# Kernel tuning notes

Hardware: AMD Instinct MI355X
Metric: run time of the kernel (lower is better)

## Reference

```python
import jax, jax.numpy as jnp
import numpy as np

B, N, E, DIN = 2048, 38, 4, 9
H0, H1, L0 = 256, 256, 512
EPS = 1e-5
_mask_np = np.ones((N, DIN), np.float32)
_mask_np[np.arange(0, N, 2), :] = 0.0
MASK = jnp.asarray(_mask_np)  # (N, DIN); masked rows zeroed


def _bn_relu(h, g, b):
    # h: (B, N, 1, D); BatchNorm2d(N) normalizes over (batch, H=1, W=D) per node channel
    mu = jnp.mean(h, axis=(0, 2, 3), keepdims=True)
    var = jnp.var(h, axis=(0, 2, 3), keepdims=True)  # biased var, as torch BN
    h = (h - mu) * jax.lax.rsqrt(var + EPS) * g[None, :, None, None] + b[None, :, None, None]
    return jax.nn.relu(h)


def _gconv(adj, nodes, Ws, bs, We, be):
    # adj: (B, E, N, N); nodes: (B, N, 1, Din)
    out = Ws.shape[0]
    hs = nodes @ Ws.T + bs  # self term: (B, N, 1, out)
    m = (nodes @ We.T + be).reshape(nodes.shape[0], N, out, E)
    hr = jnp.einsum('bemn,bnce->bmc', adj, m)  # relational aggregation
    return hs + hr[:, :, None, :]


def _forward(adj, x, cWs0, cbs0, cWe0, cbe0, cg0, cb0, cWs1, cbs1, cWe1, cbe1, cg1, cb1, lW0, lb0, lg0, lbb0, fW, fb):
    masked_x = MASK * x
    h = masked_x[:, :, None, :]
    h = _bn_relu(_gconv(adj, h, cWs0, cbs0, cWe0, cbe0), cg0, cb0)
    h = _bn_relu(_gconv(adj, h, cWs1, cbs1, cWe1, cbe1), cg1, cb1)
    h = _bn_relu(h @ lW0.T + lb0, lg0, lbb0)
    h = (h @ fW.T + fb)[:, :, 0, :]  # (B, N, 2*DIN)
    s_logits, t = h[..., :DIN], h[..., DIN:]
    s = jax.nn.sigmoid(s_logits)
    out = masked_x + (1.0 - MASK) * (x + t) * s
    logdet = jnp.sum(jax.nn.log_sigmoid(s_logits).reshape(x.shape[0], -1), axis=1)
    return out, logdet


def setup_inputs() -> dict:
    key = jax.random.key(0)
    ks = jax.random.split(key, 8)
    rn = lambda k, shape: jax.random.normal(ks[k], shape, jnp.float32) * 0.1
    return {
        'adj': jax.random.uniform(ks[0], (B, E, N, N), jnp.float32),
        'x': jax.random.normal(ks[1], (B, N, DIN), jnp.float32),
        'cWs0': rn(2, (H0, DIN)), 'cbs0': jnp.zeros((H0,), jnp.float32),
        'cWe0': rn(3, (H0 * E, DIN)), 'cbe0': jnp.zeros((H0 * E,), jnp.float32),
        'cg0': jnp.ones((N,), jnp.float32), 'cb0': jnp.zeros((N,), jnp.float32),
        'cWs1': rn(4, (H1, H0)), 'cbs1': jnp.zeros((H1,), jnp.float32),
        'cWe1': rn(5, (H1 * E, H0)), 'cbe1': jnp.zeros((H1 * E,), jnp.float32),
        'cg1': jnp.ones((N,), jnp.float32), 'cb1': jnp.zeros((N,), jnp.float32),
        'lW0': rn(6, (L0, H1)), 'lb0': jnp.zeros((L0,), jnp.float32),
        'lg0': jnp.ones((N,), jnp.float32), 'lbb0': jnp.zeros((N,), jnp.float32),
        'fW': rn(7, (2 * DIN, L0)), 'fb': jnp.zeros((2 * DIN,), jnp.float32),
    }


def reference(adj, x, cWs0, cbs0, cWe0, cbe0, cg0, cb0, cWs1, cbs1, cWe1, cbe1, cg1, cb1, lW0, lb0, lg0, lbb0, fW, fb):
    return _forward(adj, x, cWs0, cbs0, cWe0, cbe0, cg0, cb0, cWs1, cbs1, cWe1, cbe1, cg1, cb1, lW0, lb0, lg0, lbb0, fW, fb)
```

## Files before the change

kernel.cpp:

```cpp
#include <hip/hip_runtime.h>
#include <hip/hip_bf16.h>
#include <math.h>

#define B_   2048
#define N_   38
#define E_   4
#define DIN_ 9
#define H0_  256
#define H1_  256
#define L0_  512
#define M_   (B_ * N_)

typedef short bf16x8 __attribute__((ext_vector_type(8)));
typedef float f32x4 __attribute__((ext_vector_type(4)));

struct __align__(8) bf4 { __hip_bfloat16 x, y, z, w; };

__device__ __forceinline__ float b2f(unsigned short u) {
  return __uint_as_float((unsigned)u << 16);
}
__device__ __forceinline__ unsigned short f2b(float f) {
  __hip_bfloat16 h = __float2bfloat16(f);
  return *(unsigned short*)&h;
}

__device__ __forceinline__ float rsum16(float v) {
  v += __shfl_xor(v, 1);
  v += __shfl_xor(v, 2);
  v += __shfl_xor(v, 4);
  v += __shfl_xor(v, 8);
  return v;
}

__global__ void k_build_wg0(const float* __restrict__ Ws, const float* __restrict__ bs,
                            const float* __restrict__ We, const float* __restrict__ be,
                            unsigned short* __restrict__ WT) {
  int i = blockIdx.x * 256 + threadIdx.x;
  if (i >= 256 * 96) return;
  int c = i / 96, k = i % 96;
  float v = 0.f;
  if (k < 64) {
    int e = k >> 4, f = k & 15;
    if (f < 9) v = We[(c * 4 + e) * 9 + f];
    else if (f == 9) v = be[c * 4 + e];
  } else if (k < 80) {
    int f = k - 64;
    if (f < 9) v = Ws[c * 9 + f];
    else if (f == 9) v = bs[c];
  }
  WT[i] = f2b(v);
}

__global__ void k_build_wbig(const float* __restrict__ Ws, const float* __restrict__ We,
                             unsigned short* __restrict__ WT) {
  int i = blockIdx.x * 256 + threadIdx.x;
  if (i >= 1280 * 256) return;
  int j = i / 256, f = i % 256;
  float v;
  if (j < 256) v = Ws[j * 256 + f];
  else { int jj = j - 256; int e = jj >> 8, c = jj & 255; v = We[(c * 4 + e) * 256 + f]; }
  WT[i] = f2b(v);
}

__global__ void k_build_wl(const float* __restrict__ W, unsigned short* __restrict__ WT) {
  int i = blockIdx.x * 256 + threadIdx.x;
  if (i >= 512 * 256) return;
  WT[i] = f2b(W[i]);
}

__global__ void k_build_wf(const float* __restrict__ W, unsigned short* __restrict__ WT) {
  int i = blockIdx.x * 256 + threadIdx.x;
  if (i >= 32 * 512) return;
  int r = i / 512, k = i % 512;
  WT[i] = f2b(r < 18 ? W[r * 512 + k] : 0.f);
}

__global__ __launch_bounds__(256) void k_gred(const float* __restrict__ part, int nblk,
                                              float* __restrict__ st) {
  const int j = blockIdx.x, tid = threadIdx.x;
  float s = 0.f;
  for (int i = tid; i < nblk; i += 256) s += part[(size_t)i * 76 + j];
#pragma unroll
  for (int off = 32; off; off >>= 1) s += __shfl_down(s, off);
  __shared__ float r[4];
  if ((tid & 63) == 0) r[tid >> 6] = s;
  __syncthreads();
  if (tid == 0) {
    float tot = r[0] + r[1] + r[2] + r[3];
    if (j < 38) st[j * 2] = tot;
    else st[(j - 38) * 2 + 1] = tot;
  }
}

__global__ __launch_bounds__(256) void k_gconv0(
    const float* __restrict__ adj, const float* __restrict__ x,
    const unsigned short* __restrict__ Wg0, unsigned short* __restrict__ g,
    float* __restrict__ part) {
  __shared__ __align__(16) unsigned short adjB[4 * 48 * 64];
  __shared__ __align__(16) unsigned short zB[48 * 64];
  __shared__ __align__(16) unsigned short xLA[64 * 32];
  __shared__ __align__(16) unsigned short xLB[16 * 64];
  __shared__ float lsumW[4][48], lsqW[4][48];
  const int b = blockIdx.x, t = threadIdx.x;
  const uint4 z4 = make_uint4(0, 0, 0, 0);
  for (int i = t; i < 4 * 48 * 64 / 8; i += 256) ((uint4*)adjB)[i] = z4;
  for (int i = t; i < 64 * 32 / 8; i += 256) ((uint4*)xLA)[i] = z4;
  for (int i = t; i < 16 * 64 / 8; i += 256) ((uint4*)xLB)[i] = z4;
  __syncthreads();
  for (int i = t; i < 4 * 38 * 38; i += 256) {
    int e = i / 1444, r = i % 1444, m = r / 38, n = r % 38;
    adjB[(e * 48 + m) * 64 + n] = f2b(adj[(size_t)b * 5776 + i]);
  }
  for (int i = t; i < 342; i += 256) {
    int m = i / 9, f = i % 9;
    float v = x[(size_t)b * 342 + i];
    unsigned short bv = f2b((m & 1) ? v : 0.f);
    xLA[m * 32 + f] = bv;
    xLB[f * 64 + m] = bv;
  }
  if (t < 38) {
    unsigned short one = f2b(1.f);
    xLA[t * 32 + 9] = one;
    xLB[9 * 64 + t] = one;
  }
  __syncthreads();
  const int w = t >> 6, L = t & 63;
  const int lrow = L & 15, quad = L >> 4;
  {
    f32x4 za[3];
#pragma unroll
    for (int mt = 0; mt < 3; ++mt) za[mt] = (f32x4){0.f, 0.f, 0.f, 0.f};
#pragma unroll
    for (int kk = 0; kk < 2; ++kk) {
      bf16x8 bb = *(const bf16x8*)&xLB[lrow * 64 + kk * 32 + quad * 8];
#pragma unroll
      for (int mt = 0; mt < 3; ++mt) {
        bf16x8 aa = *(const bf16x8*)&adjB[(w * 48 + mt * 16 + lrow) * 64 + kk * 32 + quad * 8];
        za[mt] = __builtin_amdgcn_mfma_f32_16x16x32_bf16(aa, bb, za[mt], 0, 0, 0);
      }
    }
#pragma unroll
    for (int mt = 0; mt < 3; ++mt)
#pragma unroll
      for (int reg = 0; reg < 4; ++reg)
        zB[(mt * 16 + quad * 4 + reg) * 64 + w * 16 + lrow] = f2b(za[mt][reg]);
  }
  __syncthreads();
  f32x4 acc[3][4];
#pragma unroll
  for (int mt = 0; mt < 3; ++mt)
#pragma unroll
    for (int nt = 0; nt < 4; ++nt) acc[mt][nt] = (f32x4){0.f, 0.f, 0.f, 0.f};
#pragma unroll
  for (int kc = 0; kc < 3; ++kc) {
    bf16x8 af[3];
#pragma unroll
    for (int mt = 0; mt < 3; ++mt)
      af[mt] = (kc < 2)
                   ? *(const bf16x8*)&zB[(mt * 16 + lrow) * 64 + kc * 32 + quad * 8]
                   : *(const bf16x8*)&xLA[(mt * 16 + lrow) * 32 + quad * 8];
#pragma unroll
    for (int nt = 0; nt < 4; ++nt) {
      const int c = w * 64 + nt * 16 + lrow;
      bf16x8 bf_ = *(const bf16x8*)&Wg0[(size_t)c * 96 + kc * 32 + quad * 8];
#pragma unroll
      for (int mt = 0; mt < 3; ++mt)
        acc[mt][nt] = __builtin_amdgcn_mfma_f32_16x16x32_bf16(af[mt], bf_, acc[mt][nt], 0, 0, 0);
    }
  }
#pragma unroll
  for (int mt = 0; mt < 3; ++mt) {
#pragma unroll
    for (int reg = 0; reg < 4; ++reg) {
      const int m = mt * 16 + quad * 4 + reg;
      float sv = 0.f, qv = 0.f;
      if (m < N_) {
#pragma unroll
        for (int nt = 0; nt < 4; ++nt) {
          const int c = w * 64 + nt * 16 + lrow;
          float v = acc[mt][nt][reg];
          g[((size_t)b * N_ + m) * 256 + c] = f2b(v);
          sv += v;
          qv += v * v;
        }
      }
      sv = rsum16(sv);
      qv = rsum16(qv);
      if (lrow == 0) { lsumW[w][m] = sv; lsqW[w][m] = qv; }
    }
  }
  __syncthreads();
  if (t < 38) {
    part[(size_t)b * 76 + t] = lsumW[0][t] + lsumW[1][t] + lsumW[2][t] + lsumW[3][t];
    part[(size_t)b * 76 + 38 + t] = lsqW[0][t] + lsqW[1][t] + lsqW[2][t] + lsqW[3][t];
  }
}

template <bool BIAS, bool STATS>
__global__ __launch_bounds__(512) void k_gemm(
    const unsigned short* __restrict__ A0, const unsigned short* __restrict__ Bw,
    const float* __restrict__ bias, const float* __restrict__ stIn,
    const float* __restrict__ gam, const float* __restrict__ bet, float cnt,
    unsigned short* __restrict__ Cout, int Cstride, float* __restrict__ part) {
  __shared__ __align__(16) unsigned short lA[128 * 32];
  __shared__ __align__(16) unsigned short lB[256 * 32];
  __shared__ float lbias[256];
  __shared__ float lsum[38], lsq[38];
  const int t = threadIdx.x;
  const int tileM = blockIdx.x, n_base = blockIdx.y * 256;
  if (BIAS && t < 256) lbias[t] = bias[n_base + t];
  if (STATS && t < 38) { lsum[t] = 0.f; lsq[t] = 0.f; }
  const int w = t >> 6, L = t & 63;
  const int wr = w >> 2, wc = w & 3;
  const int lrow = L & 15, quad = L >> 4;
  const int srow = t >> 2, sseg = (t & 3) * 8;
  const int nA = (tileM * 128 + srow) % 38;
  float aC, bC;
  {
    float mu = stIn[nA * 2] / cnt;
    float var = stIn[nA * 2 + 1] / cnt - mu * mu;
    aC = rsqrtf(var + 1e-5f) * gam[nA];
    bC = bet[nA] - mu * aC;
  }
  const unsigned short* aRow = A0 + (size_t)(tileM * 128 + srow) * 256 + sseg;
  f32x4 acc[4][4];
#pragma unroll
  for (int mt = 0; mt < 4; ++mt)
#pragma unroll
    for (int nt = 0; nt < 4; ++nt) acc[mt][nt] = (f32x4){0.f, 0.f, 0.f, 0.f};

  uint4 u = *(const uint4*)aRow;
  for (int ki = 0; ki < 8; ++ki) {
#pragma unroll
    for (int r = 0; r < 2; ++r) {
      const unsigned short* gp = Bw + (size_t)(n_base + r * 128 + srow) * 256 + ki * 32 + sseg;
      __builtin_amdgcn_global_load_lds(
          (const __attribute__((address_space(1))) void*)gp,
          (__attribute__((address_space(3))) void*)(lB + r * 4096 + w * 512), 16, 0, 0);
    }
    uint4 un = u;
    if (ki < 7) un = *(const uint4*)(aRow + (ki + 1) * 32);
    {
      uint4 o;
      unsigned* up = (unsigned*)&u;
      unsigned* op = (unsigned*)&o;
#pragma unroll
      for (int j = 0; j < 4; ++j) {
        float lo = fmaxf(fmaf(b2f((unsigned short)(up[j] & 0xffff)), aC, bC), 0.f);
        float hi = fmaxf(fmaf(b2f((unsigned short)(up[j] >> 16)), aC, bC), 0.f);
        op[j] = (unsigned)f2b(lo) | ((unsigned)f2b(hi) << 16);
      }
      *(uint4*)&lA[srow * 32 + sseg] = o;
    }
    __syncthreads();
    bf16x8 af[4], bfr[4];
#pragma unroll
    for (int mt = 0; mt < 4; ++mt)
      af[mt] = *(const bf16x8*)&lA[(wr * 64 + mt * 16 + lrow) * 32 + quad * 8];
#pragma unroll
    for (int nt = 0; nt < 4; ++nt)
      bfr[nt] = *(const bf16x8*)&lB[(wc * 64 + nt * 16 + lrow) * 32 + quad * 8];
#pragma unroll
    for (int mt = 0; mt < 4; ++mt)
#pragma unroll
      for (int nt = 0; nt < 4; ++nt)
        acc[mt][nt] = __builtin_amdgcn_mfma_f32_16x16x32_bf16(af[mt], bfr[nt], acc[mt][nt], 0, 0, 0);
    __syncthreads();
    u = un;
  }
#pragma unroll
  for (int mt = 0; mt < 4; ++mt) {
#pragma unroll
    for (int reg = 0; reg < 4; ++reg) {
      const size_t row = (size_t)tileM * 128 + wr * 64 + mt * 16 + quad * 4 + reg;
      float sv = 0.f, qv = 0.f;
#pragma unroll
      for (int nt = 0; nt < 4; ++nt) {
        const int lcol = wc * 64 + nt * 16 + lrow;
        float v = acc[mt][nt][reg];
        if (BIAS) v += lbias[lcol];
        Cout[row * Cstride + n_base + lcol] = f2b(v);
        sv += v;
        qv += v * v;
      }
      if (STATS) {
        sv = rsum16(sv);
        qv = rsum16(qv);
        if (lrow == 0) {
          int n = (int)(row % 38);
          atomicAdd(&lsum[n], sv);
          atomicAdd(&lsq[n], qv);
        }
      }
    }
  }
  if (STATS) {
    __syncthreads();
    const int blk = blockIdx.y * gridDim.x + blockIdx.x;
    if (t < 38) {
      part[(size_t)blk * 76 + t] = lsum[t];
      part[(size_t)blk * 76 + 38 + t] = lsq[t];
    }
  }
}

__global__ __launch_bounds__(256) void k_hr(
    const float* __restrict__ adj, const unsigned short* __restrict__ Y,
    const float* __restrict__ bs, const float* __restrict__ be,
    unsigned short* __restrict__ h2, int b_base, float* __restrict__ part) {
  __shared__ __align__(16) unsigned short adjE[4 * 48 * 64];
  __shared__ __align__(16) unsigned short Ybt[256 * 72];
  __shared__ float arowS[4 * 48];
  __shared__ float lsumW[4][48], lsqW[4][48];
  const int t = threadIdx.x;
  const int bl = blockIdx.x, b = b_base + bl;
  for (int i = t; i < 4 * 48 * 64 / 8; i += 256) ((uint4*)adjE)[i] = make_uint4(0, 0, 0, 0);
#pragma unroll
  for (int n = 38; n < 64; ++n) Ybt[t * 72 + n] = 0;
  __syncthreads();
  for (int i = t; i < 4 * 38 * 38; i += 256) {
    int e = i / 1444, r = i % 1444, m = r / 38, n = r % 38;
    adjE[(e * 48 + m) * 64 + n] = f2b(adj[(size_t)b * 5776 + i]);
  }
  __syncthreads();
  if (t < 152) {
    int e = t / 38, m = t % 38;
    float s = 0.f;
    for (int n = 0; n < 38; ++n) s += b2f(adjE[(e * 48 + m) * 64 + n]);
    arowS[e * 48 + m] = s;
  }
  const int w = t >> 6, L = t & 63;
  const int lrow = L & 15, quad = L >> 4;
  f32x4 acc[3][4];
#pragma unroll
  for (int mt = 0; mt < 3; ++mt)
#pragma unroll
    for (int nt = 0; nt < 4; ++nt) acc[mt][nt] = (f32x4){0.f, 0.f, 0.f, 0.f};
#pragma unroll 1
  for (int e = 0; e < 4; ++e) {
    __syncthreads();
    {
      const unsigned short* yp = Y + (size_t)bl * 38 * 1280 + 256 + e * 256 + t;
#pragma unroll
      for (int n = 0; n < 38; ++n) Ybt[t * 72 + n] = yp[(size_t)n * 1280];
    }
    __syncthreads();
#pragma unroll
    for (int kk = 0; kk < 2; ++kk) {
      bf16x8 bb[4];
#pragma unroll
      for (int nt = 0; nt < 4; ++nt)
        bb[nt] = *(const bf16x8*)&Ybt[(w * 64 + nt * 16 + lrow) * 72 + kk * 32 + quad * 8];
#pragma unroll
      for (int mt = 0; mt < 3; ++mt) {
        bf16x8 aa = *(const bf16x8*)&adjE[(e * 48 + mt * 16 + lrow) * 64 + kk * 32 + quad * 8];
#pragma unroll
        for (int nt = 0; nt < 4; ++nt)
          acc[mt][nt] = __builtin_amdgcn_mfma_f32_16x16x32_bf16(aa, bb[nt], acc[mt][nt], 0, 0, 0);
      }
    }
  }
#pragma unroll
  for (int mt = 0; mt < 3; ++mt) {
#pragma unroll
    for (int reg = 0; reg < 4; ++reg) {
      const int m = mt * 16 + quad * 4 + reg;
      float sv = 0.f, qv = 0.f;
      if (m < N_) {
        float a0 = arowS[0 * 48 + m], a1 = arowS[1 * 48 + m];
        float a2 = arowS[2 * 48 + m], a3 = arowS[3 * 48 + m];
#pragma unroll
        for (int nt = 0; nt < 4; ++nt) {
          const int col = w * 64 + nt * 16 + lrow;
          float hs = b2f(Y[(size_t)(bl * 38 + m) * 1280 + col]);
          float4 bev = *(const float4*)&be[col * 4];
          float v = acc[mt][nt][reg] + hs + bs[col] +
                    a0 * bev.x + a1 * bev.y + a2 * bev.z + a3 * bev.w;
          h2[((size_t)b * N_ + m) * 256 + col] = f2b(v);
          sv += v;
          qv += v * v;
        }
      }
      sv = rsum16(sv);
      qv = rsum16(qv);
      if (lrow == 0) { lsumW[w][m] = sv; lsqW[w][m] = qv; }
    }
  }
  __syncthreads();
  if (t < 38) {
    part[(size_t)b * 76 + t] = lsumW[0][t] + lsumW[1][t] + lsumW[2][t] + lsumW[3][t];
    part[(size_t)b * 76 + 38 + t] = lsqW[0][t] + lsqW[1][t] + lsqW[2][t] + lsqW[3][t];
  }
}

__global__ __launch_bounds__(256) void k_final(
    const unsigned short* __restrict__ g2, const float* __restrict__ x,
    const unsigned short* __restrict__ Wfb, const float* __restrict__ fb,
    const float* __restrict__ st, const float* __restrict__ gam,
    const float* __restrict__ bet, float* __restrict__ out) {
  __shared__ __align__(16) unsigned short hA[48 * 520];
  __shared__ float lgS[48 * 20];
  __shared__ float aS[N_], bS[N_], fbS[20], red[4];
  const int b = blockIdx.x, tid = threadIdx.x;
  if (tid < N_) {
    const float cnt = 2048.f * 512.f;
    float mu = st[tid * 2] / cnt;
    float var = st[tid * 2 + 1] / cnt - mu * mu;
    float a = rsqrtf(var + 1e-5f) * gam[tid];
    aS[tid] = a;
    bS[tid] = bet[tid] - mu * a;
  }
  if (tid >= 64 && tid < 82) fbS[tid - 64] = fb[tid - 64];
  __syncthreads();
  for (int i = tid; i < N_ * 64; i += 256) {
    int n = i >> 6, seg = (i & 63) * 8;
    uint4 u = *(const uint4*)&g2[((size_t)b * N_ + n) * 512 + seg];
    float a = aS[n], bb = bS[n];
    float v[8];
    v[0] = b2f((unsigned short)(u.x & 0xffff)); v[1] = b2f((unsigned short)(u.x >> 16));
    v[2] = b2f((unsigned short)(u.y & 0xffff)); v[3] = b2f((unsigned short)(u.y >> 16));
    v[4] = b2f((unsigned short)(u.z & 0xffff)); v[5] = b2f((unsigned short)(u.z >> 16));
    v[6] = b2f((unsigned short)(u.w & 0xffff)); v[7] = b2f((unsigned short)(u.w >> 16));
#pragma unroll
    for (int j = 0; j < 8; ++j) v[j] = fmaxf(fmaf(v[j], a, bb), 0.f);
    uint4 o;
    o.x = (unsigned)f2b(v[0]) | ((unsigned)f2b(v[1]) << 16);
    o.y = (unsigned)f2b(v[2]) | ((unsigned)f2b(v[3]) << 16);
    o.z = (unsigned)f2b(v[4]) | ((unsigned)f2b(v[5]) << 16);
    o.w = (unsigned)f2b(v[6]) | ((unsigned)f2b(v[7]) << 16);
    *(uint4*)&hA[n * 520 + seg] = o;
  }
  for (int i = tid; i < 10 * 64; i += 256) {
    int n = 38 + (i >> 6), seg = (i & 63) * 8;
    *(uint4*)&hA[n * 520 + seg] = make_uint4(0, 0, 0, 0);
  }
  __syncthreads();
  const int w = tid >> 6, L = tid & 63;
  const int lrow = L & 15, quad = L >> 4;
  if (w < 3) {
    f32x4 acc0 = (f32x4){0.f, 0.f, 0.f, 0.f}, acc1 = (f32x4){0.f, 0.f, 0.f, 0.f};
#pragma unroll
    for (int ki = 0; ki < 16; ++ki) {
      bf16x8 af = *(const bf16x8*)&hA[(w * 16 + lrow) * 520 + ki * 32 + quad * 8];
      bf16x8 b0 = *(const bf16x8*)&Wfb[(size_t)lrow * 512 + ki * 32 + quad * 8];
      bf16x8 b1 = *(const bf16x8*)&Wfb[(size_t)(16 + lrow) * 512 + ki * 32 + quad * 8];
      acc0 = __builtin_amdgcn_mfma_f32_16x16x32_bf16(af, b0, acc0, 0, 0, 0);
      acc1 = __builtin_amdgcn_mfma_f32_16x16x32_bf16(af, b1, acc1, 0, 0, 0);
    }
#pragma unroll
    for (int reg = 0; reg < 4; ++reg) {
      int m = w * 16 + quad * 4 + reg;
      if (m < N_) {
        lgS[m * 20 + lrow] = acc0[reg] + fbS[lrow];
        if (lrow < 2) lgS[m * 20 + 16 + lrow] = acc1[reg] + fbS[16 + lrow];
      }
    }
  }
  __syncthreads();
  float ls = 0.f;
  for (int ii = tid; ii < 342; ii += 256) {
    int mm = ii / 9, d = ii % 9;
    float sl = lgS[mm * 20 + d];
    float tv = lgS[mm * 20 + 9 + d];
    float xv = x[((size_t)b * N_ + mm) * 9 + d];
    float sg = 1.f / (1.f + expf(-sl));
    float o = (mm & 1) ? xv : (xv + tv) * sg;
    out[((size_t)b * N_ + mm) * 9 + d] = o;
    ls += (sl >= 0.f) ? -log1pf(expf(-sl)) : (sl - log1pf(expf(sl)));
  }
#pragma unroll
  for (int off = 32; off; off >>= 1) ls += __shfl_down(ls, off);
  if (L == 0) red[w] = ls;
  __syncthreads();
  if (tid == 0) out[(size_t)B_ * 342 + b] = red[0] + red[1] + red[2] + red[3];
}

extern "C" void kernel_launch(void* const* d_in, const int* in_sizes, int n_in,
                              void* d_out, int out_size, void* d_ws, size_t ws_size,
                              hipStream_t stream) {
  (void)in_sizes; (void)n_in; (void)out_size; (void)ws_size;
  const float* adj  = (const float*)d_in[0];
  const float* x    = (const float*)d_in[1];
  const float* cWs0 = (const float*)d_in[2];
  const float* cbs0 = (const float*)d_in[3];
  const float* cWe0 = (const float*)d_in[4];
  const float* cbe0 = (const float*)d_in[5];
  const float* cg0  = (const float*)d_in[6];
  const float* cb0  = (const float*)d_in[7];
  const float* cWs1 = (const float*)d_in[8];
  const float* cbs1 = (const float*)d_in[9];
  const float* cWe1 = (const float*)d_in[10];
  const float* cbe1 = (const float*)d_in[11];
  const float* cg1  = (const float*)d_in[12];
  const float* cb1  = (const float*)d_in[13];
  const float* lW0  = (const float*)d_in[14];
  const float* lb0  = (const float*)d_in[15];
  const float* lg0  = (const float*)d_in[16];
  const float* lbb0 = (const float*)d_in[17];
  const float* fW   = (const float*)d_in[18];
  const float* fb   = (const float*)d_in[19];
  float* out = (float*)d_out;

  char* p = (char*)d_ws;
  float* stats = (float*)p;                     p += 1024;
  unsigned short* Wg0  = (unsigned short*)p;    p += 256 * 96 * 2;
  unsigned short* Wfb  = (unsigned short*)p;    p += 32 * 512 * 2;
  unsigned short* Wbig = (unsigned short*)p;    p += 1280 * 256 * 2;
  unsigned short* Wl   = (unsigned short*)p;    p += 512 * 256 * 2;
  float* part0 = (float*)p;                     p += 2048 * 76 * 4;
  float* part1 = (float*)p;                     p += 2048 * 76 * 4;
  float* part2 = (float*)p;                     p += 1216 * 76 * 4;
  unsigned short* g0   = (unsigned short*)p;    p += (size_t)M_ * 256 * 2;
  unsigned short* h2   = (unsigned short*)p;    p += (size_t)M_ * 256 * 2;
  unsigned short* big  = (unsigned short*)p;
  unsigned short* Ybuf = big;
  unsigned short* g2   = big;

  float* st0 = stats;
  float* st1 = stats + 76;
  float* st2 = stats + 152;

  k_build_wg0<<<96, 256, 0, stream>>>(cWs0, cbs0, cWe0, cbe0, Wg0);
  k_build_wbig<<<1280, 256, 0, stream>>>(cWs1, cWe1, Wbig);
  k_build_wl<<<512, 256, 0, stream>>>(lW0, Wl);
  k_build_wf<<<64, 256, 0, stream>>>(fW, Wfb);

  k_gconv0<<<2048, 256, 0, stream>>>(adj, x, Wg0, g0, part0);
  k_gred<<<76, 256, 0, stream>>>(part0, 2048, st0);

  for (int hh = 0; hh < 2; ++hh) {
    k_gemm<false, false><<<dim3(304, 5), 512, 0, stream>>>(
        g0 + (size_t)hh * (M_ / 2) * 256, Wbig, (const float*)nullptr,
        st0, cg0, cb0, 2048.f * 256.f, Ybuf, 1280, (float*)nullptr);
    k_hr<<<1024, 256, 0, stream>>>(adj, Ybuf, cbs1, cbe1, h2, hh * 1024, part1);
  }
  k_gred<<<76, 256, 0, stream>>>(part1, 2048, st1);

  k_gemm<true, true><<<dim3(608, 2), 512, 0, stream>>>(
      h2, Wl, lb0, st1, cg1, cb1, 2048.f * 256.f, g2, 512, part2);
  k_gred<<<76, 256, 0, stream>>>(part2, 1216, st2);

  k_final<<<2048, 256, 0, stream>>>(g2, x, Wfb, fb, st2, lg0, lbb0, out);
}
```

Baseline: 440.4 us.

## Fuse layer-1 graph conv into per-batch kernel aggregating adjacency before weights

Replaces the split GEMM (producing a 1280-wide Y intermediate in global memory) plus the k_hr aggregation kernel with a single per-batch kernel k_l1f. It applies BN+ReLU to g0 in LDS, first computes adj_e @ P per edge type (38x38 by 38x256), then multiplies that result by the matching weight slice, so the large Y buffer is never written to or read back from HBM. It uses XOR-swizzled LDS layouts to limit bank conflicts. The trade-off is that weights are streamed from global/L2 separately by each of the 2048 blocks instead of being reused across a tiled GEMM, there are extra syncs per edge type, and P is rounded to bf16 an extra time.

```diff
diff --git a/kernel.cpp b/kernel.cpp
--- a/kernel.cpp
+++ b/kernel.cpp
@@ -13,8 +13,6 @@
 
 typedef short bf16x8 __attribute__((ext_vector_type(8)));
 typedef float f32x4 __attribute__((ext_vector_type(4)));
-
-struct __align__(8) bf4 { __hip_bfloat16 x, y, z, w; };
 
 __device__ __forceinline__ float b2f(unsigned short u) {
   return __uint_as_float((unsigned)u << 16);
@@ -51,14 +49,14 @@
   WT[i] = f2b(v);
 }
 
-__global__ void k_build_wbig(const float* __restrict__ Ws, const float* __restrict__ We,
+__global__ void k_build_wcat(const float* __restrict__ Ws, const float* __restrict__ We,
                              unsigned short* __restrict__ WT) {
   int i = blockIdx.x * 256 + threadIdx.x;
-  if (i >= 1280 * 256) return;
-  int j = i / 256, f = i % 256;
+  if (i >= 256 * 1280) return;
+  int c = i / 1280, k = i % 1280;
   float v;
-  if (j < 256) v = Ws[j * 256 + f];
-  else { int jj = j - 256; int e = jj >> 8, c = jj & 255; v = We[(c * 4 + e) * 256 + f]; }
+  if (k < 256) v = Ws[c * 256 + k];
+  else { int kk = k - 256; int e = kk >> 8, f = kk & 255; v = We[(c * 4 + e) * 256 + f]; }
   WT[i] = f2b(v);
 }
 
@@ -180,6 +178,180 @@
           const int c = w * 64 + nt * 16 + lrow;
           float v = acc[mt][nt][reg];
           g[((size_t)b * N_ + m) * 256 + c] = f2b(v);
+          sv += v;
+          qv += v * v;
+        }
+      }
+      sv = rsum16(sv);
+      qv = rsum16(qv);
+      if (lrow == 0) { lsumW[w][m] = sv; lsqW[w][m] = qv; }
+    }
+  }
+  __syncthreads();
+  if (t < 38) {
+    part[(size_t)b * 76 + t] = lsumW[0][t] + lsumW[1][t] + lsumW[2][t] + lsumW[3][t];
+    part[(size_t)b * 76 + 38 + t] = lsqW[0][t] + lsqW[1][t] + lsqW[2][t] + lsqW[3][t];
+  }
+}
+
+__global__ __launch_bounds__(256) void k_l1f(
+    const float* __restrict__ adj, const unsigned short* __restrict__ g0,
+    const unsigned short* __restrict__ Wcat, const float* __restrict__ st0,
+    const float* __restrict__ gam, const float* __restrict__ bet,
+    const float* __restrict__ bs, const float* __restrict__ be,
+    unsigned short* __restrict__ h2, float* __restrict__ part) {
+  __shared__ __align__(16) unsigned short adjB[4 * 48 * 64];
+  __shared__ __align__(16) unsigned short Abt[256 * 48 + 16];
+  __shared__ __align__(16) unsigned short Pbuf[48 * 256];
+  __shared__ float aS[38], bS[38];
+  __shared__ float arowS[4 * 48];
+  __shared__ float lsumW[4][48], lsqW[4][48];
+  const int b = blockIdx.x, t = threadIdx.x;
+  for (int i = t; i < 4 * 48 * 64 / 8; i += 256) ((uint4*)adjB)[i] = make_uint4(0, 0, 0, 0);
+  if (t < 38) {
+    const float cnt = 2048.f * 256.f;
+    float mu = st0[t * 2] / cnt;
+    float var = st0[t * 2 + 1] / cnt - mu * mu;
+    float a = rsqrtf(var + 1e-5f) * gam[t];
+    aS[t] = a;
+    bS[t] = bet[t] - mu * a;
+  }
+  __syncthreads();
+  for (int i = t; i < 4 * 38 * 38; i += 256) {
+    int e = i / 1444, r = i % 1444, m = r / 38, n = r % 38;
+    *(unsigned short*)((char*)adjB + (e * 48 + m) * 128 + ((2 * n) ^ ((m & 7) << 4))) =
+        f2b(adj[(size_t)b * 5776 + i]);
+  }
+  for (int i = t; i < 38 * 32; i += 256) {
+    int n = i >> 5, seg = (i & 31) * 8;
+    uint4 u = *(const uint4*)&g0[((size_t)b * N_ + n) * 256 + seg];
+    float a = aS[n], bb2 = bS[n];
+    unsigned* up = (unsigned*)&u;
+    uint4 o;
+    unsigned* op = (unsigned*)&o;
+#pragma unroll
+    for (int j = 0; j < 4; ++j) {
+      float lo = fmaxf(fmaf(b2f((unsigned short)(up[j] & 0xffff)), a, bb2), 0.f);
+      float hi = fmaxf(fmaf(b2f((unsigned short)(up[j] >> 16)), a, bb2), 0.f);
+      op[j] = (unsigned)f2b(lo) | ((unsigned)f2b(hi) << 16);
+    }
+    *(uint4*)((char*)Pbuf + n * 512 + ((seg * 2) ^ ((n & 7) << 4))) = o;
+  }
+  for (int i = t; i < 10 * 32; i += 256) {
+    int n = 38 + (i >> 5), seg = (i & 31) * 8;
+    *(uint4*)((char*)Pbuf + n * 512 + ((seg * 2) ^ ((n & 7) << 4))) = make_uint4(0, 0, 0, 0);
+  }
+  __syncthreads();
+  if (t < 152) {
+    int e = t / 38, m = t % 38;
+    float s = 0.f;
+    for (int n = 0; n < 38; ++n)
+      s += b2f(*(const unsigned short*)((const char*)adjB + (e * 48 + m) * 128 +
+                                        ((2 * n) ^ ((m & 7) << 4))));
+    arowS[e * 48 + m] = s;
+  }
+  {
+    const int c = t;
+#pragma unroll
+    for (int j = 0; j < 5; ++j) {
+      uint4 o;
+      unsigned* op = (unsigned*)&o;
+#pragma unroll
+      for (int q = 0; q < 4; ++q) {
+        int n0 = j * 8 + q * 2;
+        unsigned short lo = 0, hi = 0;
+        if (n0 < 38)
+          lo = *(const unsigned short*)((const char*)Pbuf + n0 * 512 +
+                                        ((2 * c) ^ ((n0 & 7) << 4)));
+        if (n0 + 1 < 38)
+          hi = *(const unsigned short*)((const char*)Pbuf + (n0 + 1) * 512 +
+                                        ((2 * c) ^ (((n0 + 1) & 7) << 4)));
+        op[q] = (unsigned)lo | ((unsigned)hi << 16);
+      }
+      *(uint4*)&Abt[c * 48 + j * 8] = o;
+    }
+    *(uint4*)&Abt[c * 48 + 40] = make_uint4(0, 0, 0, 0);
+  }
+  const int w = t >> 6, L = t & 63;
+  const int lrow = L & 15, quad = L >> 4;
+  f32x4 acc[3][4];
+#pragma unroll
+  for (int mt = 0; mt < 3; ++mt)
+#pragma unroll
+    for (int nt = 0; nt < 4; ++nt) acc[mt][nt] = (f32x4){0.f, 0.f, 0.f, 0.f};
+
+#define MAIN_KBLOCK(WOFF)                                                              \
+  _Pragma("unroll") for (int kc = 0; kc < 8; ++kc) {                                   \
+    bf16x8 af[3];                                                                      \
+    _Pragma("unroll") for (int mt = 0; mt < 3; ++mt) af[mt] =                          \
+        *(const bf16x8*)((const char*)Pbuf + (mt * 16 + lrow) * 512 +                  \
+                         ((kc * 64 + quad * 16) ^ ((lrow & 7) << 4)));                 \
+    _Pragma("unroll") for (int nt = 0; nt < 4; ++nt) {                                 \
+      const int c = w * 64 + nt * 16 + lrow;                                           \
+      bf16x8 bf_ = *(const bf16x8*)&Wcat[(size_t)c * 1280 + (WOFF) + kc * 32 + quad * 8]; \
+      _Pragma("unroll") for (int mt = 0; mt < 3; ++mt) acc[mt][nt] =                   \
+          __builtin_amdgcn_mfma_f32_16x16x32_bf16(af[mt], bf_, acc[mt][nt], 0, 0, 0);  \
+    }                                                                                  \
+  }
+
+  MAIN_KBLOCK(0)
+
+#pragma unroll 1
+  for (int e = 0; e < 4; ++e) {
+    f32x4 pa[3][4];
+#pragma unroll
+    for (int mt = 0; mt < 3; ++mt)
+#pragma unroll
+      for (int nt = 0; nt < 4; ++nt) pa[mt][nt] = (f32x4){0.f, 0.f, 0.f, 0.f};
+#pragma unroll
+    for (int kk = 0; kk < 2; ++kk) {
+      bf16x8 bb[4];
+#pragma unroll
+      for (int nt = 0; nt < 4; ++nt)
+        bb[nt] = *(const bf16x8*)&Abt[(w * 64 + nt * 16 + lrow) * 48 + kk * 32 + quad * 8];
+#pragma unroll
+      for (int mt = 0; mt < 3; ++mt) {
+        bf16x8 aa = *(const bf16x8*)((const char*)adjB + (e * 48 + mt * 16 + lrow) * 128 +
+                                     ((kk * 64 + quad * 16) ^ ((lrow & 7) << 4)));
+#pragma unroll
+        for (int nt = 0; nt < 4; ++nt)
+          pa[mt][nt] = __builtin_amdgcn_mfma_f32_16x16x32_bf16(aa, bb[nt], pa[mt][nt], 0, 0, 0);
+      }
+    }
+    __syncthreads();
+#pragma unroll
+    for (int mt = 0; mt < 3; ++mt)
+#pragma unroll
+      for (int reg = 0; reg < 4; ++reg) {
+        const int m = mt * 16 + quad * 4 + reg;
+#pragma unroll
+        for (int nt = 0; nt < 4; ++nt) {
+          const int c2 = w * 64 + nt * 16 + lrow;
+          *(unsigned short*)((char*)Pbuf + m * 512 + ((2 * c2) ^ ((m & 7) << 4))) =
+              f2b(pa[mt][nt][reg]);
+        }
+      }
+    __syncthreads();
+    MAIN_KBLOCK(256 + e * 256)
+  }
+#undef MAIN_KBLOCK
+
+#pragma unroll
+  for (int mt = 0; mt < 3; ++mt) {
+#pragma unroll
+    for (int reg = 0; reg < 4; ++reg) {
+      const int m = mt * 16 + quad * 4 + reg;
+      float sv = 0.f, qv = 0.f;
+      if (m < N_) {
+        float a0 = arowS[0 * 48 + m], a1 = arowS[48 + m];
+        float a2 = arowS[96 + m], a3 = arowS[144 + m];
+#pragma unroll
+        for (int nt = 0; nt < 4; ++nt) {
+          const int col = w * 64 + nt * 16 + lrow;
+          float4 bev = *(const float4*)&be[col * 4];
+          float v = acc[mt][nt][reg] + bs[col] +
+                    a0 * bev.x + a1 * bev.y + a2 * bev.z + a3 * bev.w;
+          h2[((size_t)b * N_ + m) * 256 + col] = f2b(v);
           sv += v;
           qv += v * v;
         }
@@ -304,95 +476,6 @@
   }
 }
 
-__global__ __launch_bounds__(256) void k_hr(
-    const float* __restrict__ adj, const unsigned short* __restrict__ Y,
-    const float* __restrict__ bs, const float* __restrict__ be,
-    unsigned short* __restrict__ h2, int b_base, float* __restrict__ part) {
-  __shared__ __align__(16) unsigned short adjE[4 * 48 * 64];
-  __shared__ __align__(16) unsigned short Ybt[256 * 72];
-  __shared__ float arowS[4 * 48];
-  __shared__ float lsumW[4][48], lsqW[4][48];
-  const int t = threadIdx.x;
-  const int bl = blockIdx.x, b = b_base + bl;
-  for (int i = t; i < 4 * 48 * 64 / 8; i += 256) ((uint4*)adjE)[i] = make_uint4(0, 0, 0, 0);
-#pragma unroll
-  for (int n = 38; n < 64; ++n) Ybt[t * 72 + n] = 0;
-  __syncthreads();
-  for (int i = t; i < 4 * 38 * 38; i += 256) {
-    int e = i / 1444, r = i % 1444, m = r / 38, n = r % 38;
-    adjE[(e * 48 + m) * 64 + n] = f2b(adj[(size_t)b * 5776 + i]);
-  }
-  __syncthreads();
-  if (t < 152) {
-    int e = t / 38, m = t % 38;
-    float s = 0.f;
-    for (int n = 0; n < 38; ++n) s += b2f(adjE[(e * 48 + m) * 64 + n]);
-    arowS[e * 48 + m] = s;
-  }
-  const int w = t >> 6, L = t & 63;
-  const int lrow = L & 15, quad = L >> 4;
-  f32x4 acc[3][4];
-#pragma unroll
-  for (int mt = 0; mt < 3; ++mt)
-#pragma unroll
-    for (int nt = 0; nt < 4; ++nt) acc[mt][nt] = (f32x4){0.f, 0.f, 0.f, 0.f};
-#pragma unroll 1
-  for (int e = 0; e < 4; ++e) {
-    __syncthreads();
-    {
-      const unsigned short* yp = Y + (size_t)bl * 38 * 1280 + 256 + e * 256 + t;
-#pragma unroll
-      for (int n = 0; n < 38; ++n) Ybt[t * 72 + n] = yp[(size_t)n * 1280];
-    }
-    __syncthreads();
-#pragma unroll
-    for (int kk = 0; kk < 2; ++kk) {
-      bf16x8 bb[4];
-#pragma unroll
-      for (int nt = 0; nt < 4; ++nt)
-        bb[nt] = *(const bf16x8*)&Ybt[(w * 64 + nt * 16 + lrow) * 72 + kk * 32 + quad * 8];
-#pragma unroll
-      for (int mt = 0; mt < 3; ++mt) {
-        bf16x8 aa = *(const bf16x8*)&adjE[(e * 48 + mt * 16 + lrow) * 64 + kk * 32 + quad * 8];
-#pragma unroll
-        for (int nt = 0; nt < 4; ++nt)
-          acc[mt][nt] = __builtin_amdgcn_mfma_f32_16x16x32_bf16(aa, bb[nt], acc[mt][nt], 0, 0, 0);
-      }
-    }
-  }
-#pragma unroll
-  for (int mt = 0; mt < 3; ++mt) {
-#pragma unroll
-    for (int reg = 0; reg < 4; ++reg) {
-      const int m = mt * 16 + quad * 4 + reg;
-      float sv = 0.f, qv = 0.f;
-      if (m < N_) {
-        float a0 = arowS[0 * 48 + m], a1 = arowS[1 * 48 + m];
-        float a2 = arowS[2 * 48 + m], a3 = arowS[3 * 48 + m];
-#pragma unroll
-        for (int nt = 0; nt < 4; ++nt) {
-          const int col = w * 64 + nt * 16 + lrow;
-          float hs = b2f(Y[(size_t)(bl * 38 + m) * 1280 + col]);
-          float4 bev = *(const float4*)&be[col * 4];
-          float v = acc[mt][nt][reg] + hs + bs[col] +
-                    a0 * bev.x + a1 * bev.y + a2 * bev.z + a3 * bev.w;
-          h2[((size_t)b * N_ + m) * 256 + col] = f2b(v);
-          sv += v;
-          qv += v * v;
-        }
-      }
-      sv = rsum16(sv);
-      qv = rsum16(qv);
-      if (lrow == 0) { lsumW[w][m] = sv; lsqW[w][m] = qv; }
-    }
-  }
-  __syncthreads();
-  if (t < 38) {
-    part[(size_t)b * 76 + t] = lsumW[0][t] + lsumW[1][t] + lsumW[2][t] + lsumW[3][t];
-    part[(size_t)b * 76 + 38 + t] = lsqW[0][t] + lsqW[1][t] + lsqW[2][t] + lsqW[3][t];
-  }
-}
-
 __global__ __launch_bounds__(256) void k_final(
     const unsigned short* __restrict__ g2, const float* __restrict__ x,
     const unsigned short* __restrict__ Wfb, const float* __restrict__ fb,
@@ -505,35 +588,28 @@
   float* stats = (float*)p;                     p += 1024;
   unsigned short* Wg0  = (unsigned short*)p;    p += 256 * 96 * 2;
   unsigned short* Wfb  = (unsigned short*)p;    p += 32 * 512 * 2;
-  unsigned short* Wbig = (unsigned short*)p;    p += 1280 * 256 * 2;
+  unsigned short* Wcat = (unsigned short*)p;    p += 256 * 1280 * 2;
   unsigned short* Wl   = (unsigned short*)p;    p += 512 * 256 * 2;
   float* part0 = (float*)p;                     p += 2048 * 76 * 4;
   float* part1 = (float*)p;                     p += 2048 * 76 * 4;
   float* part2 = (float*)p;                     p += 1216 * 76 * 4;
   unsigned short* g0   = (unsigned short*)p;    p += (size_t)M_ * 256 * 2;
   unsigned short* h2   = (unsigned short*)p;    p += (size_t)M_ * 256 * 2;
-  unsigned short* big  = (unsigned short*)p;
-  unsigned short* Ybuf = big;
-  unsigned short* g2   = big;
+  unsigned short* g2   = (unsigned short*)p;
 
   float* st0 = stats;
   float* st1 = stats + 76;
   float* st2 = stats + 152;
 
   k_build_wg0<<<96, 256, 0, stream>>>(cWs0, cbs0, cWe0, cbe0, Wg0);
-  k_build_wbig<<<1280, 256, 0, stream>>>(cWs1, cWe1, Wbig);
+  k_build_wcat<<<1280, 256, 0, stream>>>(cWs1, cWe1, Wcat);
   k_build_wl<<<512, 256, 0, stream>>>(lW0, Wl);
   k_build_wf<<<64, 256, 0, stream>>>(fW, Wfb);
 
   k_gconv0<<<2048, 256, 0, stream>>>(adj, x, Wg0, g0, part0);
   k_gred<<<76, 256, 0, stream>>>(part0, 2048, st0);
 
-  for (int hh = 0; hh < 2; ++hh) {
-    k_gemm<false, false><<<dim3(304, 5), 512, 0, stream>>>(
-        g0 + (size_t)hh * (M_ / 2) * 256, Wbig, (const float*)nullptr,
-        st0, cg0, cb0, 2048.f * 256.f, Ybuf, 1280, (float*)nullptr);
-    k_hr<<<1024, 256, 0, stream>>>(adj, Ybuf, cbs1, cbe1, h2, hh * 1024, part1);
-  }
+  k_l1f<<<2048, 256, 0, stream>>>(adj, g0, Wcat, st0, cg0, cb0, cbs1, cbe1, h2, part1);
   k_gred<<<76, 256, 0, stream>>>(part1, 2048, st1);
 
   k_gemm<true, true><<<dim3(608, 2), 512, 0, stream>>>(
```

Result: slower. 454.6 us (+3.2%).
